# Kernel tuning notes

Hardware: AMD Instinct MI355X
Metric: run time of the kernel (lower is better)

## Reference

```python
import jax, jax.numpy as jnp
import numpy as np

B, S, D, H = 8, 1024, 768, 12
DH = D // H  # 64
EPS = 1e-12
NEG_INF = -1e30


def setup_inputs() -> dict:
    key = jax.random.key(0)
    ks = jax.random.split(key, 12)
    s = 0.02
    return {
        "hidden_states": jax.random.normal(ks[0], (B, S, D), jnp.float32),
        "attention_mask": jax.random.randint(ks[1], (B, 1, 1, S), 0, 2, jnp.int32),
        "Wq": jax.random.normal(ks[2], (D, D), jnp.float32) * s,
        "bq": jnp.zeros((D,), jnp.float32),
        "Wk": jax.random.normal(ks[3], (D, D), jnp.float32) * s,
        "bk": jnp.zeros((D,), jnp.float32),
        "Wv": jax.random.normal(ks[4], (D, D), jnp.float32) * s,
        "bv": jnp.zeros((D,), jnp.float32),
        "Wo": jax.random.normal(ks[5], (D, D), jnp.float32) * s,
        "bo": jnp.zeros((D,), jnp.float32),
        "ln_g": jnp.ones((D,), jnp.float32),
        "ln_b": jnp.zeros((D,), jnp.float32),
    }


def _split_heads(x):
    # [B,S,D] -> [B,H,S,DH]
    return x.reshape(B, S, H, DH).transpose(0, 2, 1, 3)


def reference(hidden_states, attention_mask, Wq, bq, Wk, bk, Wv, bv, Wo, bo, ln_g, ln_b):
    q = _split_heads(hidden_states @ Wq.T + bq)
    k = _split_heads(hidden_states @ Wk.T + bk)
    v = _split_heads(hidden_states @ Wv.T + bv)

    # scores: [B,H,S,S]
    scores = jnp.einsum("bhqd,bhkd->bhqk", q, k) / jnp.float32(np.sqrt(DH))
    mask0 = attention_mask == 0  # [B,1,1,S], broadcasts over heads/queries
    scores = jnp.where(mask0, NEG_INF, scores)
    probs = jax.nn.softmax(scores, axis=-1)
    # post-softmax masking (as in source)
    probs = jnp.where(mask0, 0.0, probs)

    ctx = jnp.einsum("bhqk,bhkd->bhqd", probs, v)
    ctx = ctx.transpose(0, 2, 1, 3).reshape(B, S, D)

    # BertSelfOutput: dense + residual + LayerNorm
    h = ctx @ Wo.T + bo + hidden_states
    mu = jnp.mean(h, axis=-1, keepdims=True)
    var = jnp.mean((h - mu) ** 2, axis=-1, keepdims=True)
    out = (h - mu) * jax.lax.rsqrt(var + EPS) * ln_g + ln_b
    return out, probs
```

## Files before the change

### kernel.cpp

```cpp
#include <hip/hip_runtime.h>

#define B_ 8
#define S_ 1024
#define D_ 768
#define H_ 12
#define DH_ 64

typedef __attribute__((ext_vector_type(8))) short short8;
typedef __attribute__((ext_vector_type(4))) short short4v;
typedef __attribute__((ext_vector_type(4))) float float4v;
typedef __attribute__((ext_vector_type(8))) __bf16 bf16x8;

static __device__ __forceinline__ short f2bf(float f) {
  union { float f; unsigned u; } v; v.f = f;
  unsigned r = v.u + 0x7fffu + ((v.u >> 16) & 1u);
  return (short)(r >> 16);
}
static __device__ __forceinline__ float bf2f(short s) {
  union { unsigned u; float f; } v; v.u = ((unsigned)(unsigned short)s) << 16;
  return v.f;
}

static __device__ __forceinline__ float4v mfma16(const short* ap, const short* bp, float4v c) {
  bf16x8 a = *(const bf16x8*)ap;
  bf16x8 b = *(const bf16x8*)bp;
  return __builtin_amdgcn_mfma_f32_16x16x32_bf16(a, b, c, 0, 0, 0);
}

typedef const __attribute__((address_space(1))) unsigned gu32;
typedef __attribute__((address_space(3))) unsigned lu32;
static __device__ __forceinline__ void gload16(const void* g, void* l) {
  __builtin_amdgcn_global_load_lds((gu32*)g, (lu32*)l, 16, 0, 0);
}

__global__ __launch_bounds__(256) void cvt_bf16(const float* __restrict__ src,
                                                short* __restrict__ dst, int n4) {
  int i = blockIdx.x * 256 + threadIdx.x;
  if (i < n4) {
    float4v v = ((const float4v*)src)[i];
    short4v o;
    o.x = f2bf(v.x); o.y = f2bf(v.y); o.z = f2bf(v.z); o.w = f2bf(v.w);
    ((short4v*)dst)[i] = o;
  }
}

__global__ __launch_bounds__(256) void cvt_w4(const float* __restrict__ w0,
                                              const float* __restrict__ w1,
                                              const float* __restrict__ w2,
                                              const float* __restrict__ w3,
                                              short* __restrict__ wqkv,
                                              short* __restrict__ wob) {
  int seg = blockIdx.x / 576, loc = blockIdx.x % 576;
  const float* src = (seg == 0) ? w0 : (seg == 1) ? w1 : (seg == 2) ? w2 : w3;
  short* dst = (seg < 3) ? (wqkv + (size_t)seg * 589824) : wob;
  int i = loc * 256 + threadIdx.x;
  float4v v = ((const float4v*)src)[i];
  short4v o;
  o.x = f2bf(v.x); o.y = f2bf(v.y); o.z = f2bf(v.z); o.w = f2bf(v.w);
  ((short4v*)dst)[i] = o;
}

__global__ __launch_bounds__(256) void gemm_qkv(const short* __restrict__ A,
                                                const short* __restrict__ Bw,
                                                const float* __restrict__ bq,
                                                const float* __restrict__ bk,
                                                const float* __restrict__ bv,
                                                short* __restrict__ Qb,
                                                short* __restrict__ Kb,
                                                short* __restrict__ Vtb) {
  __shared__ char smem[34816];
  short (*As)[32] = (short(*)[32])smem;
  short (*Bs)[32] = (short(*)[32])(smem + 8192);
  short (*Cs)[136] = (short(*)[136])smem;

  int m0 = blockIdx.x * 128, n0 = blockIdx.y * 128;
  int t = threadIdx.x, w = t >> 6, lane = t & 63;
  int wm = (w >> 1) * 64, wn = (w & 1) * 64;
  int lr = lane & 15, lk = (lane >> 4) * 8;

  const short* gA = A + (size_t)(m0 + w * 32 + (lane >> 2)) * 768 + (lane & 3) * 8;
  const short* gB = Bw + (size_t)(n0 + w * 32 + (lane >> 2)) * 768 + (lane & 3) * 8;

  float4v acc[4][4] = {};

  for (int k0 = 0; k0 < 768; k0 += 32) {
    gload16(gA, &As[w * 32][0]);
    gload16(gA + 16 * 768, &As[w * 32 + 16][0]);
    gload16(gB, &Bs[w * 32][0]);
    gload16(gB + 16 * 768, &Bs[w * 32 + 16][0]);
    gA += 32; gB += 32;
    __syncthreads();
    short8 a[4], b[4];
#pragma unroll
    for (int i = 0; i < 4; i++) a[i] = *(const short8*)&As[wm + i * 16 + lr][lk];
#pragma unroll
    for (int j = 0; j < 4; j++) b[j] = *(const short8*)&Bs[wn + j * 16 + lr][lk];
#pragma unroll
    for (int i = 0; i < 4; i++)
#pragma unroll
      for (int j = 0; j < 4; j++)
        acc[i][j] = mfma16((const short*)&a[i], (const short*)&b[j], acc[i][j]);
    __syncthreads();
  }

  int proj = blockIdx.y / 6;
  int nloc0 = n0 - proj * 768;
  int hhb = nloc0 >> 6;
  int b = m0 >> 10, s0v = m0 & 1023;

  if (proj < 2) {
    short* dst = (proj == 0) ? Qb : Kb;
    const float* bias = (proj == 0) ? bq : bk;
#pragma unroll
    for (int j = 0; j < 4; j++) {
      float bb = bias[nloc0 + wn + j * 16 + lr];
#pragma unroll
      for (int i = 0; i < 4; i++)
#pragma unroll
        for (int jj = 0; jj < 4; jj++)
          Cs[wm + i * 16 + (lane >> 4) * 4 + jj][wn + j * 16 + lr] = f2bf(acc[i][j][jj] + bb);
    }
    __syncthreads();
#pragma unroll
    for (int hh2 = 0; hh2 < 2; hh2++) {
      short* base = dst + ((size_t)(b * 12 + hhb + hh2) * 1024 + s0v) * 64;
#pragma unroll
      for (int u = 0; u < 4; u++) {
        int c = t + u * 256;
        int sl = c >> 3, dh0 = (c & 7) * 8;
        *(short8*)&base[(size_t)c * 8] = *(const short8*)&Cs[sl][hh2 * 64 + dh0];
      }
    }
  } else {
#pragma unroll
    for (int j = 0; j < 4; j++) {
      float bb = bv[nloc0 + wn + j * 16 + lr];
#pragma unroll
      for (int i = 0; i < 4; i++) {
        short4v p;
        p.x = f2bf(acc[i][j][0] + bb);
        p.y = f2bf(acc[i][j][1] + bb);
        p.z = f2bf(acc[i][j][2] + bb);
        p.w = f2bf(acc[i][j][3] + bb);
        *(short4v*)&Cs[wn + j * 16 + lr][wm + i * 16 + (lane >> 4) * 4] = p;
      }
    }
    __syncthreads();
#pragma unroll
    for (int u = 0; u < 8; u++) {
      int row = (t >> 4) + u * 16;
      int hh2 = row >> 6, dh = row & 63;
      *(short8*)&Vtb[((size_t)(b * 12 + hhb + hh2) * 64 + dh) * 1024 + s0v + (t & 15) * 8]
          = *(const short8*)&Cs[row][(t & 15) * 8];
    }
  }
}

__global__ __launch_bounds__(256) void attn_fused(const short* __restrict__ Qb,
                                                  const short* __restrict__ Kb,
                                                  const short* __restrict__ Vtb,
                                                  const int* __restrict__ amask,
                                                  float* __restrict__ probs,
                                                  short* __restrict__ ctxb) {
  __shared__ short P[16][1032];
  __shared__ float ctxf[16][68];
  __shared__ float redmax[4][16];
  __shared__ float redsum[4][16];

  int qt = blockIdx.x, bh = blockIdx.y;
  int b = bh / 12, h = bh - b * 12;
  int q0 = qt * 16;
  const short* Qp = Qb + ((size_t)bh * 1024 + q0) * 64;
  const short* Kp = Kb + (size_t)bh * 65536;
  const short* Vp = Vtb + (size_t)bh * 65536;
  const int* mb = amask + b * 1024;

  int t = threadIdx.x, w = t >> 6, lane = t & 63;
  int lr = lane & 15, lg = lane >> 4, lk = lg * 8;

  short8 aq0 = *(const short8*)&Qp[lr * 64 + lk];
  short8 aq1 = *(const short8*)&Qp[lr * 64 + 32 + lk];

  float4v acc[16] = {};
#pragma unroll
  for (int nt = 0; nt < 16; nt++) {
    const short* kp = Kp + (size_t)(w * 256 + nt * 16 + lr) * 64;
    short8 b0 = *(const short8*)&kp[lk];
    short8 b1 = *(const short8*)&kp[32 + lk];
    acc[nt] = mfma16((const short*)&aq0, (const short*)&b0, acc[nt]);
    acc[nt] = mfma16((const short*)&aq1, (const short*)&b1, acc[nt]);
  }

  unsigned mbits = 0;
#pragma unroll
  for (int nt = 0; nt < 16; nt++)
    mbits |= (mb[w * 256 + nt * 16 + lr] != 0 ? 1u : 0u) << nt;

  float mx[4] = {-1e30f, -1e30f, -1e30f, -1e30f};
#pragma unroll
  for (int nt = 0; nt < 16; nt++)
#pragma unroll
    for (int j = 0; j < 4; j++) {
      float s = acc[nt][j] * 0.125f;
      if (!((mbits >> nt) & 1)) s = -1e30f;
      acc[nt][j] = s;
      mx[j] = fmaxf(mx[j], s);
    }
#pragma unroll
  for (int j = 0; j < 4; j++) {
#pragma unroll
    for (int off = 1; off < 16; off <<= 1) mx[j] = fmaxf(mx[j], __shfl_xor(mx[j], off));
  }
  if (lr == 0) {
#pragma unroll
    for (int j = 0; j < 4; j++) redmax[w][lg * 4 + j] = mx[j];
  }
  __syncthreads();
  float gmx[4];
#pragma unroll
  for (int j = 0; j < 4; j++) {
    int r = lg * 4 + j;
    gmx[j] = fmaxf(fmaxf(redmax[0][r], redmax[1][r]), fmaxf(redmax[2][r], redmax[3][r]));
  }

  float sm[4] = {0.f, 0.f, 0.f, 0.f};
#pragma unroll
  for (int nt = 0; nt < 16; nt++)
#pragma unroll
    for (int j = 0; j < 4; j++) {
      float p = ((mbits >> nt) & 1) ? __expf(acc[nt][j] - gmx[j]) : 0.f;
      acc[nt][j] = p;
      sm[j] += p;
    }
#pragma unroll
  for (int j = 0; j < 4; j++) {
#pragma unroll
    for (int off = 1; off < 16; off <<= 1) sm[j] += __shfl_xor(sm[j], off);
  }
  if (lr == 0) {
#pragma unroll
    for (int j = 0; j < 4; j++) redsum[w][lg * 4 + j] = sm[j];
  }
  __syncthreads();
  float inv[4];
#pragma unroll
  for (int j = 0; j < 4; j++) {
    int r = lg * 4 + j;
    float s = redsum[0][r] + redsum[1][r] + redsum[2][r] + redsum[3][r];
    inv[j] = (s > 0.f) ? 1.f / s : 0.f;
  }

#pragma unroll
  for (int nt = 0; nt < 16; nt++) {
    int col = w * 256 + nt * 16 + lr;
#pragma unroll
    for (int j = 0; j < 4; j++)
      P[lg * 4 + j][col] = f2bf(acc[nt][j] * inv[j]);
  }
  __syncthreads();

  size_t pbase = ((size_t)bh * 1024 + q0) * 1024;
  {
    int prow = t >> 4;
    int cb = (t & 15) * 4;
    float* orow = probs + pbase + (size_t)prow * 1024;
#pragma unroll
    for (int u = 0; u < 16; u++) {
      int col = cb + u * 64;
      short4v pv = *(const short4v*)&P[prow][col];
      float4v f;
      f.x = bf2f(pv.x); f.y = bf2f(pv.y); f.z = bf2f(pv.z); f.w = bf2f(pv.w);
      *(float4v*)&orow[col] = f;
    }
  }

  float4v c0 = {}, c1 = {};
  const short* vrow = Vp + (size_t)(w * 16 + lr) * 1024;
#pragma unroll
  for (int kk = 0; kk < 32; kk += 2) {
    short8 ap0 = *(const short8*)&P[lr][kk * 32 + lk];
    short8 bv0 = *(const short8*)&vrow[kk * 32 + lk];
    c0 = mfma16((const short*)&ap0, (const short*)&bv0, c0);
    short8 ap1 = *(const short8*)&P[lr][(kk + 1) * 32 + lk];
    short8 bv1 = *(const short8*)&vrow[(kk + 1) * 32 + lk];
    c1 = mfma16((const short*)&ap1, (const short*)&bv1, c1);
  }
  c0 = c0 + c1;
#pragma unroll
  for (int j = 0; j < 4; j++)
    ctxf[lg * 4 + j][w * 16 + lr] = c0[j];
  __syncthreads();

  if (t < 128) {
    int row = t >> 3, g = t & 7;
    const float* src = &ctxf[row][g * 8];
    short8 o;
    o[0] = f2bf(src[0]); o[1] = f2bf(src[1]); o[2] = f2bf(src[2]); o[3] = f2bf(src[3]);
    o[4] = f2bf(src[4]); o[5] = f2bf(src[5]); o[6] = f2bf(src[6]); o[7] = f2bf(src[7]);
    *(short8*)&ctxb[((size_t)(b * 1024 + q0 + row)) * 768 + h * 64 + g * 8] = o;
  }
}

__global__ __launch_bounds__(256) void gemm_o(const short* __restrict__ A,
                                              const short* __restrict__ Bw,
                                              const float* __restrict__ bo,
                                              const float* __restrict__ hidden,
                                              float* __restrict__ hout) {
  __shared__ short As[128][32];
  __shared__ short Bs[128][32];
  int m0 = blockIdx.x * 128, n0 = blockIdx.y * 128;
  int t = threadIdx.x, w = t >> 6, lane = t & 63;
  int wm = (w >> 1) * 64, wn = (w & 1) * 64;
  int lr = lane & 15, lk = (lane >> 4) * 8;

  const short* gA = A + (size_t)(m0 + w * 32 + (lane >> 2)) * 768 + (lane & 3) * 8;
  const short* gB = Bw + (size_t)(n0 + w * 32 + (lane >> 2)) * 768 + (lane & 3) * 8;

  float4v acc[4][4] = {};

  for (int k0 = 0; k0 < 768; k0 += 32) {
    gload16(gA, &As[w * 32][0]);
    gload16(gA + 16 * 768, &As[w * 32 + 16][0]);
    gload16(gB, &Bs[w * 32][0]);
    gload16(gB + 16 * 768, &Bs[w * 32 + 16][0]);
    gA += 32; gB += 32;
    __syncthreads();
    short8 a[4], b[4];
#pragma unroll
    for (int i = 0; i < 4; i++) a[i] = *(const short8*)&As[wm + i * 16 + lr][lk];
#pragma unroll
    for (int j = 0; j < 4; j++) b[j] = *(const short8*)&Bs[wn + j * 16 + lr][lk];
#pragma unroll
    for (int i = 0; i < 4; i++)
#pragma unroll
      for (int j = 0; j < 4; j++)
        acc[i][j] = mfma16((const short*)&a[i], (const short*)&b[j], acc[i][j]);
    __syncthreads();
  }

#pragma unroll
  for (int j = 0; j < 4; j++) {
    int gn = n0 + wn + j * 16 + lr;
    float bb = bo[gn];
#pragma unroll
    for (int i = 0; i < 4; i++) {
      int gm0 = m0 + wm + i * 16 + ((lane >> 4) << 2);
#pragma unroll
      for (int jj = 0; jj < 4; jj++) {
        int r = gm0 + jj;
        size_t idx = (size_t)r * 768 + gn;
        hout[idx] = acc[i][j][jj] + bb + hidden[idx];
      }
    }
  }
}

__global__ __launch_bounds__(256) void lnorm(const float* __restrict__ h,
                                             const float* __restrict__ g,
                                             const float* __restrict__ be,
                                             float* __restrict__ out) {
  int row = blockIdx.x;
  const float* x = h + (size_t)row * 768;
  int t = threadIdx.x;
  float v0 = x[t], v1 = x[t + 256], v2 = x[t + 512];
  float s = v0 + v1 + v2;
#pragma unroll
  for (int off = 1; off < 64; off <<= 1) s += __shfl_xor(s, off);
  __shared__ float r1[4], r2[4];
  if ((t & 63) == 0) r1[t >> 6] = s;
  __syncthreads();
  float mean = (r1[0] + r1[1] + r1[2] + r1[3]) * (1.f / 768.f);
  float d0 = v0 - mean, d1 = v1 - mean, d2 = v2 - mean;
  float q = d0 * d0 + d1 * d1 + d2 * d2;
#pragma unroll
  for (int off = 1; off < 64; off <<= 1) q += __shfl_xor(q, off);
  if ((t & 63) == 0) r2[t >> 6] = q;
  __syncthreads();
  float var = (r2[0] + r2[1] + r2[2] + r2[3]) * (1.f / 768.f);
  float rr = rsqrtf(var + 1e-12f);
  size_t o = (size_t)row * 768;
  out[o + t]       = d0 * rr * g[t] + be[t];
  out[o + t + 256] = d1 * rr * g[t + 256] + be[t + 256];
  out[o + t + 512] = d2 * rr * g[t + 512] + be[t + 512];
}

extern "C" void kernel_launch(void* const* d_in, const int* in_sizes, int n_in,
                              void* d_out, int out_size, void* d_ws, size_t ws_size,
                              hipStream_t stream) {
  const float* hs    = (const float*)d_in[0];
  const int*   amask = (const int*)d_in[1];
  const float* Wq    = (const float*)d_in[2];
  const float* bq    = (const float*)d_in[3];
  const float* Wk    = (const float*)d_in[4];
  const float* bk    = (const float*)d_in[5];
  const float* Wv    = (const float*)d_in[6];
  const float* bv    = (const float*)d_in[7];
  const float* Wo    = (const float*)d_in[8];
  const float* bo    = (const float*)d_in[9];
  const float* lng   = (const float*)d_in[10];
  const float* lnb   = (const float*)d_in[11];

  char* wsp = (char*)d_ws;
  const size_t NTOK = (size_t)B_ * S_;
  short* hsb  = (short*)wsp; wsp += NTOK * D_ * 2;
  short* wqkv = (short*)wsp; wsp += (size_t)3 * D_ * D_ * 2;
  short* wob  = (short*)wsp; wsp += (size_t)D_ * D_ * 2;
  short* Qb   = (short*)wsp; wsp += NTOK * D_ * 2;
  short* Kb   = (short*)wsp; wsp += NTOK * D_ * 2;
  short* Vtb  = (short*)wsp; wsp += NTOK * D_ * 2;
  short* ctxb = (short*)wsp; wsp += NTOK * D_ * 2;
  float* hbuf = (float*)wsp; wsp += NTOK * D_ * 4;

  float* out   = (float*)d_out;
  float* probs = out + NTOK * D_;

  int n4hs = (int)(NTOK * D_ / 4);
  cvt_bf16<<<dim3((n4hs + 255) / 256), dim3(256), 0, stream>>>(hs, hsb, n4hs);
  cvt_w4<<<dim3(4 * 576), dim3(256), 0, stream>>>(Wq, Wk, Wv, Wo, wqkv, wob);

  gemm_qkv<<<dim3(64, 18), dim3(256), 0, stream>>>(hsb, wqkv, bq, bk, bv, Qb, Kb, Vtb);
  attn_fused<<<dim3(64, 96), dim3(256), 0, stream>>>(Qb, Kb, Vtb, amask, probs, ctxb);
  gemm_o<<<dim3(64, 6), dim3(256), 0, stream>>>(ctxb, wob, bo, hs, hbuf);
  lnorm<<<dim3(8192), dim3(256), 0, stream>>>(hbuf, lng, lnb, out);
}
```

Baseline: 718.6 us.

## Remap attention blocks per XCD, stream probs nontemporally, vectorize layernorm

Attention now uses a 1D grid and remaps each block index so that the blocks landing on the same XCD (index mod 8) work on consecutive query tiles of the same batch-head. This is meant to improve K/V reuse in each XCD's L2. The large fp32 probs tensor is written with nontemporal stores so it does less cache pollution. LayerNorm is rewritten for 192 threads, each loading and storing one float4, which cuts instruction count and yields wider memory transactions.

New measurement: 680.4 us. 5.3% less time.

```diff
diff --git a/kernel.cpp b/kernel.cpp
--- a/kernel.cpp
+++ b/kernel.cpp
@@ -167,7 +167,9 @@
   __shared__ float redmax[4][16];
   __shared__ float redsum[4][16];
 
-  int qt = blockIdx.x, bh = blockIdx.y;
+  int orig = blockIdx.x;
+  int g = (orig & 7) * 768 + (orig >> 3);
+  int bh = g >> 6, qt = g & 63;
   int b = bh / 12, h = bh - b * 12;
   int q0 = qt * 16;
   const short* Qp = Qb + ((size_t)bh * 1024 + q0) * 64;
@@ -270,7 +272,7 @@
       short4v pv = *(const short4v*)&P[prow][col];
       float4v f;
       f.x = bf2f(pv.x); f.y = bf2f(pv.y); f.z = bf2f(pv.z); f.w = bf2f(pv.w);
-      *(float4v*)&orow[col] = f;
+      __builtin_nontemporal_store(f, (float4v*)&orow[col]);
     }
   }
 
@@ -292,12 +294,12 @@
   __syncthreads();
 
   if (t < 128) {
-    int row = t >> 3, g = t & 7;
-    const float* src = &ctxf[row][g * 8];
+    int row = t >> 3, gg = t & 7;
+    const float* src = &ctxf[row][gg * 8];
     short8 o;
     o[0] = f2bf(src[0]); o[1] = f2bf(src[1]); o[2] = f2bf(src[2]); o[3] = f2bf(src[3]);
     o[4] = f2bf(src[4]); o[5] = f2bf(src[5]); o[6] = f2bf(src[6]); o[7] = f2bf(src[7]);
-    *(short8*)&ctxb[((size_t)(b * 1024 + q0 + row)) * 768 + h * 64 + g * 8] = o;
+    *(short8*)&ctxb[((size_t)(b * 1024 + q0 + row)) * 768 + h * 64 + gg * 8] = o;
   }
 }
 
@@ -355,33 +357,38 @@
   }
 }
 
-__global__ __launch_bounds__(256) void lnorm(const float* __restrict__ h,
+__global__ __launch_bounds__(192) void lnorm(const float* __restrict__ h,
                                              const float* __restrict__ g,
                                              const float* __restrict__ be,
                                              float* __restrict__ out) {
   int row = blockIdx.x;
-  const float* x = h + (size_t)row * 768;
   int t = threadIdx.x;
-  float v0 = x[t], v1 = x[t + 256], v2 = x[t + 512];
-  float s = v0 + v1 + v2;
+  const float4v* x4 = (const float4v*)(h + (size_t)row * 768);
+  float4v v = x4[t];
+  float s = v.x + v.y + v.z + v.w;
 #pragma unroll
   for (int off = 1; off < 64; off <<= 1) s += __shfl_xor(s, off);
-  __shared__ float r1[4], r2[4];
+  __shared__ float r1[3], r2[3];
   if ((t & 63) == 0) r1[t >> 6] = s;
   __syncthreads();
-  float mean = (r1[0] + r1[1] + r1[2] + r1[3]) * (1.f / 768.f);
-  float d0 = v0 - mean, d1 = v1 - mean, d2 = v2 - mean;
-  float q = d0 * d0 + d1 * d1 + d2 * d2;
+  float mean = (r1[0] + r1[1] + r1[2]) * (1.f / 768.f);
+  float4v d;
+  d.x = v.x - mean; d.y = v.y - mean; d.z = v.z - mean; d.w = v.w - mean;
+  float q = d.x * d.x + d.y * d.y + d.z * d.z + d.w * d.w;
 #pragma unroll
   for (int off = 1; off < 64; off <<= 1) q += __shfl_xor(q, off);
   if ((t & 63) == 0) r2[t >> 6] = q;
   __syncthreads();
-  float var = (r2[0] + r2[1] + r2[2] + r2[3]) * (1.f / 768.f);
+  float var = (r2[0] + r2[1] + r2[2]) * (1.f / 768.f);
   float rr = rsqrtf(var + 1e-12f);
-  size_t o = (size_t)row * 768;
-  out[o + t]       = d0 * rr * g[t] + be[t];
-  out[o + t + 256] = d1 * rr * g[t + 256] + be[t + 256];
-  out[o + t + 512] = d2 * rr * g[t + 512] + be[t + 512];
+  float4v g4 = ((const float4v*)g)[t];
+  float4v b4 = ((const float4v*)be)[t];
+  float4v o;
+  o.x = d.x * rr * g4.x + b4.x;
+  o.y = d.y * rr * g4.y + b4.y;
+  o.z = d.z * rr * g4.z + b4.z;
+  o.w = d.w * rr * g4.w + b4.w;
+  ((float4v*)(out + (size_t)row * 768))[t] = o;
 }
 
 extern "C" void kernel_launch(void* const* d_in, const int* in_sizes, int n_in,
@@ -419,7 +426,7 @@
   cvt_w4<<<dim3(4 * 576), dim3(256), 0, stream>>>(Wq, Wk, Wv, Wo, wqkv, wob);
 
   gemm_qkv<<<dim3(64, 18), dim3(256), 0, stream>>>(hsb, wqkv, bq, bk, bv, Qb, Kb, Vtb);
-  attn_fused<<<dim3(64, 96), dim3(256), 0, stream>>>(Qb, Kb, Vtb, amask, probs, ctxb);
+  attn_fused<<<dim3(6144), dim3(256), 0, stream>>>(Qb, Kb, Vtb, amask, probs, ctxb);
   gemm_o<<<dim3(64, 6), dim3(256), 0, stream>>>(ctxb, wob, bo, hs, hbuf);
-  lnorm<<<dim3(8192), dim3(256), 0, stream>>>(hbuf, lng, lnb, out);
-}
+  lnorm<<<dim3(8192), dim3(192), 0, stream>>>(hbuf, lng, lnb, out);
+}
```
